# Optimization experiments

Hardware: AMD Instinct MI355X
Metric: run time of the kernel (lower is better)

Reference implementation:

```python
import jax, jax.numpy as jnp
import numpy as np

VAR0, VAR1 = 0.1, 0.2
THRESHOLD = 0.35
NEGPOS_RATIO = 7
LOW_GT_THRESH = 0.2  # match() filters GT whose best prior IoU < 0.2


def setup_inputs() -> dict:
    key = jax.random.key(0)
    ks = jax.random.split(key, 8)
    B, P, G = 16, 43008, 128
    loc_data = jax.random.normal(ks[0], (B, P, 4), jnp.float32)
    conf_data = jax.random.normal(ks[1], (B, P, 2), jnp.float32)
    landm_data = jax.random.normal(ks[2], (B, P, 10), jnp.float32)
    # priors in cxcywh form, positive sizes
    pc = jax.random.uniform(ks[3], (P, 2), jnp.float32)
    pwh = jax.random.uniform(ks[4], (P, 2), jnp.float32, minval=0.02, maxval=0.32)
    priors = jnp.concatenate([pc, pwh], axis=1)
    # targets: valid xyxy boxes + 10 landmark coords + label (face=1)
    ctr = jax.random.uniform(ks[5], (B, G, 2), jnp.float32, minval=0.2, maxval=0.8)
    wh = jax.random.uniform(ks[6], (B, G, 2), jnp.float32, minval=0.05, maxval=0.3)
    boxes = jnp.concatenate([ctr - wh / 2, ctr + wh / 2], axis=-1)
    landms = jax.random.uniform(ks[7], (B, G, 10), jnp.float32)
    labels = jnp.ones((B, G, 1), jnp.float32)
    targets = jnp.concatenate([boxes, landms, labels], axis=-1)
    return {"loc_data": loc_data, "conf_data": conf_data, "landm_data": landm_data,
            "priors": priors, "targets": targets}


def point_form(priors):
    return jnp.concatenate([priors[:, :2] - priors[:, 2:] / 2,
                            priors[:, :2] + priors[:, 2:] / 2], axis=1)


def jaccard(a, b):  # a: [G,4] xyxy, b: [P,4] xyxy -> [G,P]
    lt = jnp.maximum(a[:, None, :2], b[None, :, :2])
    rb = jnp.minimum(a[:, None, 2:], b[None, :, 2:])
    wh = jnp.clip(rb - lt, 0.0)
    inter = wh[..., 0] * wh[..., 1]
    area_a = (a[:, 2] - a[:, 0]) * (a[:, 3] - a[:, 1])
    area_b = (b[:, 2] - b[:, 0]) * (b[:, 3] - b[:, 1])
    return inter / (area_a[:, None] + area_b[None, :] - inter)


def encode(matched, priors):  # matched xyxy [P,4], priors cxcywh [P,4]
    g_cxcy = (matched[:, :2] + matched[:, 2:]) / 2 - priors[:, :2]
    g_cxcy = g_cxcy / (VAR0 * priors[:, 2:])
    g_wh = jnp.log((matched[:, 2:] - matched[:, :2]) / priors[:, 2:]) / VAR1
    return jnp.concatenate([g_cxcy, g_wh], axis=1)


def encode_landm(matched, priors):  # matched [P,10], priors [P,4]
    m = matched.reshape(-1, 5, 2)
    g = (m - priors[:, None, :2]) / (VAR0 * priors[:, None, 2:])
    return g.reshape(-1, 10)


def match_one(truths, labels, landms, priors):
    G = truths.shape[0]
    overlaps = jaccard(truths, point_form(priors))  # [G, P]
    best_prior_overlap = overlaps.max(axis=1)       # [G]
    best_prior_idx = overlaps.argmax(axis=1)        # [G]
    valid = best_prior_overlap >= LOW_GT_THRESH
    any_valid = jnp.any(valid)
    best_truth_overlap = overlaps.max(axis=0)       # [P]
    best_truth_idx = overlaps.argmax(axis=0)        # [P]
    # index_fill_(0, best_prior_idx_filter, 2): ensure each valid GT keeps its best prior
    fill_val = jnp.where(valid, 2.0, best_truth_overlap[best_prior_idx])
    best_truth_overlap = best_truth_overlap.at[best_prior_idx].set(fill_val)
    # best_truth_idx[best_prior_idx[j]] = j for all j
    best_truth_idx = best_truth_idx.at[best_prior_idx].set(jnp.arange(G))
    matches = truths[best_truth_idx]                       # [P,4]
    conf = labels[best_truth_idx].astype(jnp.int32)        # [P]
    conf = jnp.where(best_truth_overlap < THRESHOLD, 0, conf)
    conf = jnp.where(any_valid, conf, 0)  # no valid GT -> all background
    loc = encode(matches, priors)
    landm = encode_landm(landms[best_truth_idx], priors)
    return loc, conf, landm


def smooth_l1(x):
    ax = jnp.abs(x)
    return jnp.where(ax < 1.0, 0.5 * ax * ax, ax - 0.5)


def reference(loc_data, conf_data, landm_data, priors, targets):
    truths = targets[..., :4]
    landms = targets[..., 4:14]
    labels = targets[..., 14]
    loc_t, conf_t, landm_t = jax.vmap(
        lambda t, l, lm: match_one(t, l, lm, priors))(truths, labels, landms)

    # landmark loss over positives
    pos1 = conf_t > 0
    N1 = jnp.maximum(pos1.sum().astype(jnp.float32), 1.0)
    loss_landm = jnp.sum(smooth_l1(landm_data - landm_t) * pos1[..., None])

    # localization loss over positives
    pos = conf_t != 0
    num_pos = pos.sum(axis=1, keepdims=True)  # [B,1]
    loss_l = jnp.sum(smooth_l1(loc_data - loc_t) * pos[..., None])

    # hard negative mining on per-prior CE loss
    lse = jax.scipy.special.logsumexp(conf_data, axis=-1)  # [B,P]
    gathered = jnp.take_along_axis(conf_data, conf_t[..., None], axis=-1)[..., 0]
    ce_all = lse - gathered                                # [B,P] per-prior CE
    mine = jnp.where(pos, 0.0, ce_all)
    loss_idx = jnp.argsort(-mine, axis=1)
    idx_rank = jnp.argsort(loss_idx, axis=1)
    num_neg = jnp.clip(NEGPOS_RATIO * num_pos, None, pos.shape[1] - 1)
    neg = idx_rank < num_neg
    sel = pos | neg
    loss_c = jnp.sum(jnp.where(sel, ce_all, 0.0))

    N = jnp.maximum(num_pos.sum().astype(jnp.float32), 1.0)
    return loss_l / N, loss_c / N, loss_landm / N1
```

## Files before the change

### kernel.cpp

```cpp
#include <hip/hip_runtime.h>
#include <stdint.h>


#define GC 8
#define PPI 4

__device__ __forceinline__ float sl1(float x) {
  float a = fabsf(x);
  return a < 1.f ? 0.5f * a * a : a - 0.5f;
}

__device__ __forceinline__ double dwave(double v) {
#pragma unroll
  for (int o = 32; o; o >>= 1) v += __shfl_down(v, o);
  return v;
}

__global__ __launch_bounds__(256) void k_match(
    const float* __restrict__ priors, const float* __restrict__ targets,
    float* __restrict__ bto, int* __restrict__ bti,
    unsigned long long* __restrict__ bp, int P, int G, int NIOU, int PTI,
    int NGC, int PC) {
  int tid = threadIdx.x;
  __shared__ float4 sgt[128];
  __shared__ float sga[128];
  __shared__ unsigned long long sred[GC * 256];

  if ((int)blockIdx.x < NIOU) {
    int b = blockIdx.x / PTI, tile = blockIdx.x % PTI;
    int base = tile * (256 * PPI);
    for (int g = tid; g < G; g += 256) {
      const float* t = targets + ((size_t)b * G + g) * 15;
      float x1 = t[0], y1 = t[1], x2 = t[2], y2 = t[3];
      sgt[g] = make_float4(x1, y1, x2, y2);
      sga[g] = (x2 - x1) * (y2 - y1);
    }
    __syncthreads();

    float px1[PPI], py1[PPI], px2[PPI], py2[PPI], pa[PPI];
    float bi[PPI], sb[PPI];
    int bidx[PPI];
#pragma unroll
    for (int k = 0; k < PPI; ++k) {
      int p = base + tid + k * 256;
      int pl = p < P ? p : P - 1;
      float4 pr = ((const float4*)priors)[pl];
      px1[k] = pr.x - pr.z * 0.5f; py1[k] = pr.y - pr.w * 0.5f;
      px2[k] = pr.x + pr.z * 0.5f; py2[k] = pr.y + pr.w * 0.5f;
      pa[k] = pr.z * pr.w;
      bi[k] = 0.f; sb[k] = 1.f; bidx[k] = 0;
    }

#define IOU_BODY(T, A, GG)                                                 \
  {                                                                        \
    float iw = fminf(T.z, px2[k]) - fmaxf(T.x, px1[k]);                    \
    float ih = fminf(T.w, py2[k]) - fmaxf(T.y, py1[k]);                    \
    float inter = fmaxf(iw, 0.f) * ih;        \
    float S = A + pa[k];                                                   \
    if (inter * sb[k] > bi[k] * S) { bi[k] = inter; sb[k] = S; bidx[k] = GG; } \
  }

    for (int g = 0; g < G; g += 4) {
      float4 T0 = sgt[g], T1 = sgt[g + 1], T2 = sgt[g + 2], T3 = sgt[g + 3];
      float A0 = sga[g], A1 = sga[g + 1], A2 = sga[g + 2], A3 = sga[g + 3];
#pragma unroll
      for (int k = 0; k < PPI; ++k) {
        IOU_BODY(T0, A0, g)
        IOU_BODY(T1, A1, g + 1)
        IOU_BODY(T2, A2, g + 2)
        IOU_BODY(T3, A3, g + 3)
      }
    }
#undef IOU_BODY
#pragma unroll
    for (int k = 0; k < PPI; ++k) {
      int p = base + tid + k * 256;
      if (p < P) {
        bto[(size_t)b * P + p] = bi[k] / (sb[k] - bi[k]);
        bti[(size_t)b * P + p] = bidx[k];
      }
    }
  } else {
    int bc = blockIdx.x - NIOU;
    int pc = bc % PC;
    int gcb = (bc / PC) % NGC;
    int b = bc / (PC * NGC);
    int g0 = gcb * GC;

    if (tid < GC) {
      int g = g0 + tid;
      float4 v = make_float4(0.f, 0.f, 0.f, 0.f);
      if (g < G) {
        const float* t = targets + ((size_t)b * G + g) * 15;
        v = make_float4(t[0], t[1], t[2], t[3]);
      }
      sgt[tid] = v;
    }
    __syncthreads();

    float gx1[GC], gy1[GC], gx2[GC], gy2[GC], ga[GC];
#pragma unroll
    for (int j = 0; j < GC; ++j) {
      float4 T = sgt[j];
      gx1[j] = T.x; gy1[j] = T.y; gx2[j] = T.z; gy2[j] = T.w;
      ga[j] = (T.z - T.x) * (T.w - T.y);
    }

    int chunk = (P + PC - 1) / PC;
    int ps = pc * chunk;
    int pe = ps + chunk; if (pe > P) pe = P;
    int count = pe - ps;

    float bi[GC], sb[GC];
    unsigned bpp[GC];
#pragma unroll
    for (int j = 0; j < GC; ++j) { bi[j] = 0.f; sb[j] = 1.f; bpp[j] = (unsigned)(ps + tid); }

#define BP_BODY(X1, Y1, X2, Y2, AR, PP)                                     \
  {                                                                         \
    float iw = fminf(gx2[j], X2) - fmaxf(gx1[j], X1);                       \
    float ih = fminf(gy2[j], Y2) - fmaxf(gy1[j], Y1);                       \
    float inter = fmaxf(iw, 0.f) * ih;                                      \
    float S = ga[j] + AR;                                                   \
    if (inter * sb[j] > bi[j] * S) { bi[j] = inter; sb[j] = S; bpp[j] = (unsigned)PP; } \
  }

    for (int i = tid; i < count; i += 1024) {
      int p0 = ps + i;
      int i1 = i + 256, i2 = i + 512, i3 = i + 768;
      int p1 = (i1 < count) ? ps + i1 : p0;
      int p2 = (i2 < count) ? ps + i2 : p0;
      int p3 = (i3 < count) ? ps + i3 : p0;
      float4 q0 = ((const float4*)priors)[p0];
      float4 q1 = ((const float4*)priors)[p1];
      float4 q2 = ((const float4*)priors)[p2];
      float4 q3 = ((const float4*)priors)[p3];
      float ax1 = q0.x - q0.z * 0.5f, ay1 = q0.y - q0.w * 0.5f;
      float ax2 = q0.x + q0.z * 0.5f, ay2 = q0.y + q0.w * 0.5f;
      float aa = q0.z * q0.w;
      float bx1 = q1.x - q1.z * 0.5f, by1 = q1.y - q1.w * 0.5f;
      float bx2 = q1.x + q1.z * 0.5f, by2 = q1.y + q1.w * 0.5f;
      float ba = q1.z * q1.w;
      float cx1 = q2.x - q2.z * 0.5f, cy1 = q2.y - q2.w * 0.5f;
      float cx2 = q2.x + q2.z * 0.5f, cy2 = q2.y + q2.w * 0.5f;
      float ca = q2.z * q2.w;
      float dx1 = q3.x - q3.z * 0.5f, dy1 = q3.y - q3.w * 0.5f;
      float dx2 = q3.x + q3.z * 0.5f, dy2 = q3.y + q3.w * 0.5f;
      float da = q3.z * q3.w;
#pragma unroll
      for (int j = 0; j < GC; ++j) {
        BP_BODY(ax1, ay1, ax2, ay2, aa, p0)
        BP_BODY(bx1, by1, bx2, by2, ba, p1)
        BP_BODY(cx1, cy1, cx2, cy2, ca, p2)
        BP_BODY(dx1, dy1, dx2, dy2, da, p3)
      }
    }
#undef BP_BODY

#pragma unroll
    for (int j = 0; j < GC; ++j) {
      float iou = bi[j] / (sb[j] - bi[j]);
      unsigned long long pk =
          ((unsigned long long)__float_as_uint(iou) << 32) | (unsigned)(~bpp[j]);
      sred[j * 256 + tid] = pk;
    }
    __syncthreads();
    {
      int j = tid >> 5, s = tid & 31;
      unsigned long long m = sred[j * 256 + s];
#pragma unroll
      for (int t = 1; t < 8; ++t) {
        unsigned long long v = sred[j * 256 + s + t * 32];
        if (v > m) m = v;
      }
      __syncthreads();
      sred[j * 256 + s] = m;
    }
    __syncthreads();
    if (tid < GC) {
      unsigned long long m = sred[tid * 256];
      for (int s = 1; s < 32; ++s) {
        unsigned long long v = sred[tid * 256 + s];
        if (v > m) m = v;
      }
      int g = g0 + tid;
      if (g < G) atomicMax(&bp[(size_t)b * G + g], m);
    }
  }
}

__global__ void k_scatter(const unsigned long long* __restrict__ bp,
                          float* __restrict__ bto, int* __restrict__ bti,
                          int* __restrict__ anyv, int P, int G) {
  int b = blockIdx.x, g = threadIdx.x;
  __shared__ unsigned spp[128];
  __shared__ int s_any;
  if (g == 0) s_any = 0;
  __syncthreads();
  unsigned long long m = bp[(size_t)b * G + g];
  unsigned pp = ~(unsigned)m;
  float val = __uint_as_float((unsigned)(m >> 32));
  bool ok = (m != 0ULL);
  float oldv = 0.f;
  if (ok) oldv = bto[(size_t)b * P + pp];
  spp[g] = ok ? pp : 0xFFFFFFFFu;
  if (ok && val >= 0.2f) s_any = 1;
  __syncthreads();
  bool win = ok;
  for (int g2 = g + 1; g2 < G; ++g2)
    if (spp[g2] == pp) win = false;
  if (win) {
    bto[(size_t)b * P + pp] = (val >= 0.2f) ? 2.0f : oldv;
    bti[(size_t)b * P + pp] = g;
  }
  __syncthreads();
  if (g == 0) anyv[b] = s_any;
}

__global__ __launch_bounds__(256) void k_main(
    const float* __restrict__ loc, const float* __restrict__ conf,
    const float* __restrict__ lm, const float* __restrict__ priors,
    const float* __restrict__ targets, const float* __restrict__ bto,
    const int* __restrict__ bti, const int* __restrict__ anyv,
    float* __restrict__ mine, unsigned* __restrict__ h1,
    double* __restrict__ pll, double* __restrict__ pllm,
    double* __restrict__ plc, double* __restrict__ msum,
    int* __restrict__ pnp, int P, int G, int PT) {
  int b = blockIdx.x / PT, tile = blockIdx.x % PT;
  int tid = threadIdx.x;
  int p = tile * 256 + tid;

  __shared__ float st[128 * 15];
  __shared__ unsigned hist[1024];
  __shared__ double rs[16];
  __shared__ int ri[4];

  for (int i = tid; i < G * 15; i += 256) st[i] = targets[(size_t)b * G * 15 + i];
  for (int i = tid; i < 1024; i += 256) hist[i] = 0;
  __syncthreads();

  double ll = 0, llm = 0, lc = 0, ms = 0;
  int np = 0;
  if (p < P) {
    size_t idx = (size_t)b * P + p;
    int av = anyv[b];
    float ov = bto[idx];
    int ti = bti[idx];
    bool pos = av && (ov >= 0.35f);

    float2 c = ((const float2*)conf)[idx];
    float mx = fmaxf(c.x, c.y);
    float lse = mx + logf(expf(c.x - mx) + expf(c.y - mx));
    float ce = lse - (pos ? c.y : c.x);
    float mv = pos ? 0.f : ce;
    mine[idx] = mv;
    ms = (double)mv;
    atomicAdd(&hist[__float_as_uint(mv) >> 21], 1u);

    if (pos) {
      np = 1;
      lc = (double)ce;
      float4 pr = ((const float4*)priors)[p];
      const float* t = st + ti * 15;
      float dx = 0.1f * pr.z, dy = 0.1f * pr.w;
      float gx = ((t[0] + t[2]) * 0.5f - pr.x) / dx;
      float gy = ((t[1] + t[3]) * 0.5f - pr.y) / dy;
      float gw = logf((t[2] - t[0]) / pr.z) * 5.0f;
      float gh = logf((t[3] - t[1]) / pr.w) * 5.0f;
      float4 ld = ((const float4*)loc)[idx];
      ll = (double)(sl1(ld.x - gx) + sl1(ld.y - gy) + sl1(ld.z - gw) +
                    sl1(ld.w - gh));
      const float2* lmd = (const float2*)lm + idx * 5;
      float s = 0.f;
#pragma unroll
      for (int j = 0; j < 5; ++j) {
        float2 lv = lmd[j];
        float ex = (t[4 + 2 * j] - pr.x) / dx;
        float ey = (t[5 + 2 * j] - pr.y) / dy;
        s += sl1(lv.x - ex) + sl1(lv.y - ey);
      }
      llm = (double)s;
    }
  }

  ll = dwave(ll);
  llm = dwave(llm);
  lc = dwave(lc);
  ms = dwave(ms);
#pragma unroll
  for (int o = 32; o; o >>= 1) np += __shfl_down(np, o);
  int lane = tid & 63, wid = tid >> 6;
  if (lane == 0) {
    rs[wid] = ll; rs[4 + wid] = llm; rs[8 + wid] = lc; rs[12 + wid] = ms;
    ri[wid] = np;
  }
  __syncthreads();
  if (tid == 0) {
    pll[blockIdx.x] = rs[0] + rs[1] + rs[2] + rs[3];
    pllm[blockIdx.x] = rs[4] + rs[5] + rs[6] + rs[7];
    plc[blockIdx.x] = rs[8] + rs[9] + rs[10] + rs[11];
    msum[blockIdx.x] = rs[12] + rs[13] + rs[14] + rs[15];
    pnp[blockIdx.x] = ri[0] + ri[1] + ri[2] + ri[3];
  }
  for (int i = tid; i < 1024; i += 256)
    if (hist[i]) atomicAdd(&h1[(size_t)b * 1024 + i], hist[i]);
}

__global__ __launch_bounds__(1024) void k_tail(
    const unsigned* __restrict__ h1, const int* __restrict__ pnp,
    const double* __restrict__ msum, const float* __restrict__ mine,
    int* __restrict__ num_pos, double* __restrict__ pfs_b, int P, int PT) {
  int b = blockIdx.x, tid = threadIdx.x;
  __shared__ double sm[1024];
  __shared__ int sn[1024];
  __shared__ unsigned S[1024];
  __shared__ unsigned hs[2048];
  __shared__ int spf1, sk1, spf21, sk2;
  __shared__ unsigned stb;
  __shared__ double stie;
  __shared__ double rs[16];

  int n = 0;
  double m = 0;
  for (int i = tid; i < PT; i += 1024) { n += pnp[b * PT + i]; m += msum[b * PT + i]; }
  sn[tid] = n; sm[tid] = m;
  __syncthreads();
  for (int off = 512; off; off >>= 1) {
    if (tid < off) { sn[tid] += sn[tid + off]; sm[tid] += sm[tid + off]; }
    __syncthreads();
  }
  int npos = sn[0];
  if (tid == 0) num_pos[b] = npos;

  long long k = 7LL * (long long)npos;
  long long cap = P - 1;
  if (k <= 0) return;
  if (k >= cap) {
    if (tid == 0) pfs_b[b] = sm[0];
    return;
  }

  const float* mrow = mine + (size_t)b * P;

  {
    unsigned own = h1[(size_t)b * 1024 + tid];
    S[tid] = own;
    __syncthreads();
    for (int off = 1; off < 1024; off <<= 1) {
      unsigned add = (tid + off < 1024) ? S[tid + off] : 0;
      __syncthreads();
      S[tid] += add;
      __syncthreads();
    }
    int cnt = __syncthreads_count((long long)S[tid] >= k);
    int seg = cnt - 1;
    if (tid == seg) {
      long long cum = (seg + 1 < 1024) ? (long long)S[seg + 1] : 0;
      spf1 = seg;
      sk1 = (int)(k - cum);
    }
  }
  __syncthreads();
  int pf = spf1;

  hs[tid] = 0; hs[tid + 1024] = 0;
  __syncthreads();
  for (int base = 0; base < P; base += 4096) {
    int i0 = base + tid;
    int i1 = i0 + 1024, i2 = i0 + 2048, i3 = i0 + 3072;
    unsigned b0 = (i0 < P) ? __float_as_uint(mrow[i0]) : 0u;
    unsigned b1 = (i1 < P) ? __float_as_uint(mrow[i1]) : 0u;
    unsigned b2 = (i2 < P) ? __float_as_uint(mrow[i2]) : 0u;
    unsigned b3 = (i3 < P) ? __float_as_uint(mrow[i3]) : 0u;
    if (i0 < P && (int)(b0 >> 21) == pf) atomicAdd(&hs[(b0 >> 10) & 2047], 1u);
    if (i1 < P && (int)(b1 >> 21) == pf) atomicAdd(&hs[(b1 >> 10) & 2047], 1u);
    if (i2 < P && (int)(b2 >> 21) == pf) atomicAdd(&hs[(b2 >> 10) & 2047], 1u);
    if (i3 < P && (int)(b3 >> 21) == pf) atomicAdd(&hs[(b3 >> 10) & 2047], 1u);
  }
  __syncthreads();
  {
    unsigned h0 = hs[tid * 2], h1v = hs[tid * 2 + 1];
    S[tid] = h0 + h1v;
    __syncthreads();
    for (int off = 1; off < 1024; off <<= 1) {
      unsigned add = (tid + off < 1024) ? S[tid + off] : 0;
      __syncthreads();
      S[tid] += add;
      __syncthreads();
    }
    long long kk = (long long)sk1;
    int cnt = __syncthreads_count((long long)S[tid] >= kk);
    int seg = cnt - 1;
    if (tid == seg) {
      long long cum = (seg + 1 < 1024) ? (long long)S[seg + 1] : 0;
      int bin = seg * 2;
      if (cum + h1v >= kk) bin = seg * 2 + 1;
      else cum += h1v;
      spf21 = (pf << 11) | bin;
      sk2 = (int)(kk - cum);
    }
  }
  __syncthreads();
  int pf21 = spf21;

  hs[tid] = 0;
  __syncthreads();
  for (int base = 0; base < P; base += 4096) {
    int i0 = base + tid;
    int i1 = i0 + 1024, i2 = i0 + 2048, i3 = i0 + 3072;
    unsigned b0 = (i0 < P) ? __float_as_uint(mrow[i0]) : 0u;
    unsigned b1 = (i1 < P) ? __float_as_uint(mrow[i1]) : 0u;
    unsigned b2 = (i2 < P) ? __float_as_uint(mrow[i2]) : 0u;
    unsigned b3 = (i3 < P) ? __float_as_uint(mrow[i3]) : 0u;
    if (i0 < P && (int)(b0 >> 10) == pf21) atomicAdd(&hs[b0 & 1023], 1u);
    if (i1 < P && (int)(b1 >> 10) == pf21) atomicAdd(&hs[b1 & 1023], 1u);
    if (i2 < P && (int)(b2 >> 10) == pf21) atomicAdd(&hs[b2 & 1023], 1u);
    if (i3 < P && (int)(b3 >> 10) == pf21) atomicAdd(&hs[b3 & 1023], 1u);
  }
  __syncthreads();
  {
    unsigned own = hs[tid];
    S[tid] = own;
    __syncthreads();
    for (int off = 1; off < 1024; off <<= 1) {
      unsigned add = (tid + off < 1024) ? S[tid + off] : 0;
      __syncthreads();
      S[tid] += add;
      __syncthreads();
    }
    long long kk = (long long)sk2;
    int cnt = __syncthreads_count((long long)S[tid] >= kk);
    int seg = cnt - 1;
    if (tid == seg) {
      long long cum = (seg + 1 < 1024) ? (long long)S[seg + 1] : 0;
      unsigned tb = ((unsigned)pf21 << 10) | (unsigned)seg;
      stb = tb;
      stie = (double)(kk - cum) * (double)__uint_as_float(tb);
    }
  }
  __syncthreads();

  unsigned tb = stb;
  double v = 0.0;
  for (int base = 0; base < P; base += 4096) {
    int i0 = base + tid;
    int i1 = i0 + 1024, i2 = i0 + 2048, i3 = i0 + 3072;
    unsigned b0 = (i0 < P) ? __float_as_uint(mrow[i0]) : 0u;
    unsigned b1 = (i1 < P) ? __float_as_uint(mrow[i1]) : 0u;
    unsigned b2 = (i2 < P) ? __float_as_uint(mrow[i2]) : 0u;
    unsigned b3 = (i3 < P) ? __float_as_uint(mrow[i3]) : 0u;
    if (b0 > tb) v += (double)__uint_as_float(b0);
    if (b1 > tb) v += (double)__uint_as_float(b1);
    if (b2 > tb) v += (double)__uint_as_float(b2);
    if (b3 > tb) v += (double)__uint_as_float(b3);
  }
  v = dwave(v);
  int lane = tid & 63, wid = tid >> 6;
  if (lane == 0) rs[wid] = v;
  __syncthreads();
  if (tid == 0) {
    double t = 0;
    for (int i = 0; i < 16; ++i) t += rs[i];
    pfs_b[b] = t + stie;
  }
}

__global__ __launch_bounds__(256) void k_fin(
    const double* __restrict__ pll, const double* __restrict__ pllm,
    const double* __restrict__ plc, const double* __restrict__ pfs_b,
    const int* __restrict__ num_pos, float* __restrict__ out, int NBm, int B) {
  int tid = threadIdx.x;
  double a = 0, c = 0, d = 0, f = 0, n = 0;
  for (int i = tid; i < NBm; i += 256) { a += pll[i]; c += pllm[i]; d += plc[i]; }
  for (int i = tid; i < B; i += 256) { f += pfs_b[i]; n += (double)num_pos[i]; }
  a = dwave(a); c = dwave(c); d = dwave(d); f = dwave(f); n = dwave(n);
  __shared__ double rs[5 * 4];
  int lane = tid & 63, wid = tid >> 6;
  if (lane == 0) {
    rs[wid] = a; rs[4 + wid] = c; rs[8 + wid] = d;
    rs[12 + wid] = f; rs[16 + wid] = n;
  }
  __syncthreads();
  if (tid == 0) {
    double A = rs[0] + rs[1] + rs[2] + rs[3];
    double C = rs[4] + rs[5] + rs[6] + rs[7];
    double D = rs[8] + rs[9] + rs[10] + rs[11];
    double F = rs[12] + rs[13] + rs[14] + rs[15];
    double N = rs[16] + rs[17] + rs[18] + rs[19];
    if (N < 1.0) N = 1.0;
    out[0] = (float)(A / N);
    out[1] = (float)((D + F) / N);
    out[2] = (float)(C / N);
  }
}

extern "C" void kernel_launch(void* const* d_in, const int* in_sizes, int n_in,
                              void* d_out, int out_size, void* d_ws,
                              size_t ws_size, hipStream_t stream) {
  const float* loc = (const float*)d_in[0];
  const float* conf = (const float*)d_in[1];
  const float* lm = (const float*)d_in[2];
  const float* priors = (const float*)d_in[3];
  const float* targets = (const float*)d_in[4];

  int P = in_sizes[3] / 4;
  int B = in_sizes[0] / (4 * P);
  int G = in_sizes[4] / (15 * B);
  int PT = (P + 255) / 256;
  int PTI = (P + 256 * PPI - 1) / (256 * PPI);
  int NBm = B * PT;
  int NGC = (G + GC - 1) / GC;
  int PC = 8;
  int NIOU = B * PTI;
  int NBP = B * NGC * PC;

  char* w = (char*)d_ws;
  size_t off = 0;
  unsigned long long* bp = (unsigned long long*)(w + off);
  off += (size_t)B * G * 8;
  double* pfs_b = (double*)(w + off);
  off += (size_t)B * 8;
  int* ctrl = (int*)(w + off);
  off += (size_t)(2 * B) * 4;
  int* anyv = ctrl;
  int* num_pos = ctrl + B;
  unsigned* h1 = (unsigned*)(w + off);
  off += (size_t)B * 1024 * 4;
  size_t clear_bytes = off;
  off = (off + 255) & ~(size_t)255;
  float* bto = (float*)(w + off);
  off += (size_t)B * P * 4;
  int* bti = (int*)(w + off);
  off += (size_t)B * P * 4;
  float* mine = (float*)(w + off);
  off += (size_t)B * P * 4;
  double* pll = (double*)(w + off);
  off += (size_t)NBm * 8;
  double* pllm = (double*)(w + off);
  off += (size_t)NBm * 8;
  double* plc = (double*)(w + off);
  off += (size_t)NBm * 8;
  double* msum = (double*)(w + off);
  off += (size_t)NBm * 8;
  int* pnp = (int*)(w + off);
  off += (size_t)NBm * 4;

  hipMemsetAsync(d_ws, 0, clear_bytes, stream);

  k_match<<<NIOU + NBP, 256, 0, stream>>>(priors, targets, bto, bti, bp, P, G,
                                          NIOU, PTI, NGC, PC);
  k_scatter<<<B, G, 0, stream>>>(bp, bto, bti, anyv, P, G);
  k_main<<<B * PT, 256, 0, stream>>>(loc, conf, lm, priors, targets, bto, bti,
                                     anyv, mine, h1, pll, pllm, plc, msum, pnp,
                                     P, G, PT);
  k_tail<<<B, 1024, 0, stream>>>(h1, pnp, msum, mine, num_pos, pfs_b, P, PT);
  k_fin<<<1, 256, 0, stream>>>(pll, pllm, plc, pfs_b, num_pos, (float*)d_out,
                               NBm, B);
}
```

Before: 178.8 us.

## Split match kernel, fuse final reduction into tail, cheapen per-prior math

```diff
diff --git a/kernel.cpp b/kernel.cpp
--- a/kernel.cpp
+++ b/kernel.cpp
@@ -3,7 +3,7 @@
 
 
 #define GC 8
-#define PPI 4
+#define PPI 2
 
 __device__ __forceinline__ float sl1(float x) {
   float a = fabsf(x);
@@ -16,40 +16,36 @@
   return v;
 }
 
-__global__ __launch_bounds__(256) void k_match(
+__global__ __launch_bounds__(256) void k_iou(
     const float* __restrict__ priors, const float* __restrict__ targets,
-    float* __restrict__ bto, int* __restrict__ bti,
-    unsigned long long* __restrict__ bp, int P, int G, int NIOU, int PTI,
-    int NGC, int PC) {
+    float* __restrict__ bto, int* __restrict__ bti, int P, int G, int PTI) {
   int tid = threadIdx.x;
   __shared__ float4 sgt[128];
   __shared__ float sga[128];
-  __shared__ unsigned long long sred[GC * 256];
-
-  if ((int)blockIdx.x < NIOU) {
-    int b = blockIdx.x / PTI, tile = blockIdx.x % PTI;
-    int base = tile * (256 * PPI);
-    for (int g = tid; g < G; g += 256) {
-      const float* t = targets + ((size_t)b * G + g) * 15;
-      float x1 = t[0], y1 = t[1], x2 = t[2], y2 = t[3];
-      sgt[g] = make_float4(x1, y1, x2, y2);
-      sga[g] = (x2 - x1) * (y2 - y1);
-    }
-    __syncthreads();
-
-    float px1[PPI], py1[PPI], px2[PPI], py2[PPI], pa[PPI];
-    float bi[PPI], sb[PPI];
-    int bidx[PPI];
-#pragma unroll
-    for (int k = 0; k < PPI; ++k) {
-      int p = base + tid + k * 256;
-      int pl = p < P ? p : P - 1;
-      float4 pr = ((const float4*)priors)[pl];
-      px1[k] = pr.x - pr.z * 0.5f; py1[k] = pr.y - pr.w * 0.5f;
-      px2[k] = pr.x + pr.z * 0.5f; py2[k] = pr.y + pr.w * 0.5f;
-      pa[k] = pr.z * pr.w;
-      bi[k] = 0.f; sb[k] = 1.f; bidx[k] = 0;
-    }
+
+  int b = blockIdx.x / PTI, tile = blockIdx.x % PTI;
+  int base = tile * (256 * PPI);
+  for (int g = tid; g < G; g += 256) {
+    const float* t = targets + ((size_t)b * G + g) * 15;
+    float x1 = t[0], y1 = t[1], x2 = t[2], y2 = t[3];
+    sgt[g] = make_float4(x1, y1, x2, y2);
+    sga[g] = (x2 - x1) * (y2 - y1);
+  }
+  __syncthreads();
+
+  float px1[PPI], py1[PPI], px2[PPI], py2[PPI], pa[PPI];
+  float bi[PPI], sb[PPI];
+  int bidx[PPI];
+#pragma unroll
+  for (int k = 0; k < PPI; ++k) {
+    int p = base + tid + k * 256;
+    int pl = p < P ? p : P - 1;
+    float4 pr = ((const float4*)priors)[pl];
+    px1[k] = pr.x - pr.z * 0.5f; py1[k] = pr.y - pr.w * 0.5f;
+    px2[k] = pr.x + pr.z * 0.5f; py2[k] = pr.y + pr.w * 0.5f;
+    pa[k] = pr.z * pr.w;
+    bi[k] = 0.f; sb[k] = 1.f; bidx[k] = 0;
+  }
 
 #define IOU_BODY(T, A, GG)                                                 \
   {                                                                        \
@@ -60,61 +56,69 @@
     if (inter * sb[k] > bi[k] * S) { bi[k] = inter; sb[k] = S; bidx[k] = GG; } \
   }
 
-    for (int g = 0; g < G; g += 4) {
-      float4 T0 = sgt[g], T1 = sgt[g + 1], T2 = sgt[g + 2], T3 = sgt[g + 3];
-      float A0 = sga[g], A1 = sga[g + 1], A2 = sga[g + 2], A3 = sga[g + 3];
-#pragma unroll
-      for (int k = 0; k < PPI; ++k) {
-        IOU_BODY(T0, A0, g)
-        IOU_BODY(T1, A1, g + 1)
-        IOU_BODY(T2, A2, g + 2)
-        IOU_BODY(T3, A3, g + 3)
-      }
-    }
+  for (int g = 0; g < G; g += 4) {
+    float4 T0 = sgt[g], T1 = sgt[g + 1], T2 = sgt[g + 2], T3 = sgt[g + 3];
+    float A0 = sga[g], A1 = sga[g + 1], A2 = sga[g + 2], A3 = sga[g + 3];
+#pragma unroll
+    for (int k = 0; k < PPI; ++k) {
+      IOU_BODY(T0, A0, g)
+      IOU_BODY(T1, A1, g + 1)
+      IOU_BODY(T2, A2, g + 2)
+      IOU_BODY(T3, A3, g + 3)
+    }
+  }
 #undef IOU_BODY
 #pragma unroll
-    for (int k = 0; k < PPI; ++k) {
-      int p = base + tid + k * 256;
-      if (p < P) {
-        bto[(size_t)b * P + p] = bi[k] / (sb[k] - bi[k]);
-        bti[(size_t)b * P + p] = bidx[k];
-      }
-    }
-  } else {
-    int bc = blockIdx.x - NIOU;
-    int pc = bc % PC;
-    int gcb = (bc / PC) % NGC;
-    int b = bc / (PC * NGC);
-    int g0 = gcb * GC;
-
-    if (tid < GC) {
-      int g = g0 + tid;
-      float4 v = make_float4(0.f, 0.f, 0.f, 0.f);
-      if (g < G) {
-        const float* t = targets + ((size_t)b * G + g) * 15;
-        v = make_float4(t[0], t[1], t[2], t[3]);
-      }
-      sgt[tid] = v;
-    }
-    __syncthreads();
-
-    float gx1[GC], gy1[GC], gx2[GC], gy2[GC], ga[GC];
-#pragma unroll
-    for (int j = 0; j < GC; ++j) {
-      float4 T = sgt[j];
-      gx1[j] = T.x; gy1[j] = T.y; gx2[j] = T.z; gy2[j] = T.w;
-      ga[j] = (T.z - T.x) * (T.w - T.y);
-    }
-
-    int chunk = (P + PC - 1) / PC;
-    int ps = pc * chunk;
-    int pe = ps + chunk; if (pe > P) pe = P;
-    int count = pe - ps;
-
-    float bi[GC], sb[GC];
-    unsigned bpp[GC];
-#pragma unroll
-    for (int j = 0; j < GC; ++j) { bi[j] = 0.f; sb[j] = 1.f; bpp[j] = (unsigned)(ps + tid); }
+  for (int k = 0; k < PPI; ++k) {
+    int p = base + tid + k * 256;
+    if (p < P) {
+      bto[(size_t)b * P + p] = bi[k] / (sb[k] - bi[k]);
+      bti[(size_t)b * P + p] = bidx[k];
+    }
+  }
+}
+
+__global__ __launch_bounds__(256) void k_bp(
+    const float* __restrict__ priors, const float* __restrict__ targets,
+    unsigned long long* __restrict__ bp, int P, int G, int NGC, int PC) {
+  int tid = threadIdx.x;
+  __shared__ float4 sgt[GC];
+  __shared__ unsigned long long sred[GC * 256];
+
+  int bc = blockIdx.x;
+  int pc = bc % PC;
+  int gcb = (bc / PC) % NGC;
+  int b = bc / (PC * NGC);
+  int g0 = gcb * GC;
+
+  if (tid < GC) {
+    int g = g0 + tid;
+    float4 v = make_float4(0.f, 0.f, 0.f, 0.f);
+    if (g < G) {
+      const float* t = targets + ((size_t)b * G + g) * 15;
+      v = make_float4(t[0], t[1], t[2], t[3]);
+    }
+    sgt[tid] = v;
+  }
+  __syncthreads();
+
+  float gx1[GC], gy1[GC], gx2[GC], gy2[GC], ga[GC];
+#pragma unroll
+  for (int j = 0; j < GC; ++j) {
+    float4 T = sgt[j];
+    gx1[j] = T.x; gy1[j] = T.y; gx2[j] = T.z; gy2[j] = T.w;
+    ga[j] = (T.z - T.x) * (T.w - T.y);
+  }
+
+  int chunk = (P + PC - 1) / PC;
+  int ps = pc * chunk;
+  int pe = ps + chunk; if (pe > P) pe = P;
+  int count = pe - ps;
+
+  float bi[GC], sb[GC];
+  unsigned bpp[GC];
+#pragma unroll
+  for (int j = 0; j < GC; ++j) { bi[j] = 0.f; sb[j] = 1.f; bpp[j] = (unsigned)(ps + tid); }
 
 #define BP_BODY(X1, Y1, X2, Y2, AR, PP)                                     \
   {                                                                         \
@@ -125,67 +129,66 @@
     if (inter * sb[j] > bi[j] * S) { bi[j] = inter; sb[j] = S; bpp[j] = (unsigned)PP; } \
   }
 
-    for (int i = tid; i < count; i += 1024) {
-      int p0 = ps + i;
-      int i1 = i + 256, i2 = i + 512, i3 = i + 768;
-      int p1 = (i1 < count) ? ps + i1 : p0;
-      int p2 = (i2 < count) ? ps + i2 : p0;
-      int p3 = (i3 < count) ? ps + i3 : p0;
-      float4 q0 = ((const float4*)priors)[p0];
-      float4 q1 = ((const float4*)priors)[p1];
-      float4 q2 = ((const float4*)priors)[p2];
-      float4 q3 = ((const float4*)priors)[p3];
-      float ax1 = q0.x - q0.z * 0.5f, ay1 = q0.y - q0.w * 0.5f;
-      float ax2 = q0.x + q0.z * 0.5f, ay2 = q0.y + q0.w * 0.5f;
-      float aa = q0.z * q0.w;
-      float bx1 = q1.x - q1.z * 0.5f, by1 = q1.y - q1.w * 0.5f;
-      float bx2 = q1.x + q1.z * 0.5f, by2 = q1.y + q1.w * 0.5f;
-      float ba = q1.z * q1.w;
-      float cx1 = q2.x - q2.z * 0.5f, cy1 = q2.y - q2.w * 0.5f;
-      float cx2 = q2.x + q2.z * 0.5f, cy2 = q2.y + q2.w * 0.5f;
-      float ca = q2.z * q2.w;
-      float dx1 = q3.x - q3.z * 0.5f, dy1 = q3.y - q3.w * 0.5f;
-      float dx2 = q3.x + q3.z * 0.5f, dy2 = q3.y + q3.w * 0.5f;
-      float da = q3.z * q3.w;
-#pragma unroll
-      for (int j = 0; j < GC; ++j) {
-        BP_BODY(ax1, ay1, ax2, ay2, aa, p0)
-        BP_BODY(bx1, by1, bx2, by2, ba, p1)
-        BP_BODY(cx1, cy1, cx2, cy2, ca, p2)
-        BP_BODY(dx1, dy1, dx2, dy2, da, p3)
-      }
-    }
+  for (int i = tid; i < count; i += 1024) {
+    int p0 = ps + i;
+    int i1 = i + 256, i2 = i + 512, i3 = i + 768;
+    int p1 = (i1 < count) ? ps + i1 : p0;
+    int p2 = (i2 < count) ? ps + i2 : p0;
+    int p3 = (i3 < count) ? ps + i3 : p0;
+    float4 q0 = ((const float4*)priors)[p0];
+    float4 q1 = ((const float4*)priors)[p1];
+    float4 q2 = ((const float4*)priors)[p2];
+    float4 q3 = ((const float4*)priors)[p3];
+    float ax1 = q0.x - q0.z * 0.5f, ay1 = q0.y - q0.w * 0.5f;
+    float ax2 = q0.x + q0.z * 0.5f, ay2 = q0.y + q0.w * 0.5f;
+    float aa = q0.z * q0.w;
+    float bx1 = q1.x - q1.z * 0.5f, by1 = q1.y - q1.w * 0.5f;
+    float bx2 = q1.x + q1.z * 0.5f, by2 = q1.y + q1.w * 0.5f;
+    float ba = q1.z * q1.w;
+    float cx1 = q2.x - q2.z * 0.5f, cy1 = q2.y - q2.w * 0.5f;
+    float cx2 = q2.x + q2.z * 0.5f, cy2 = q2.y + q2.w * 0.5f;
+    float ca = q2.z * q2.w;
+    float dx1 = q3.x - q3.z * 0.5f, dy1 = q3.y - q3.w * 0.5f;
+    float dx2 = q3.x + q3.z * 0.5f, dy2 = q3.y + q3.w * 0.5f;
+    float da = q3.z * q3.w;
+#pragma unroll
+    for (int j = 0; j < GC; ++j) {
+      BP_BODY(ax1, ay1, ax2, ay2, aa, p0)
+      BP_BODY(bx1, by1, bx2, by2, ba, p1)
+      BP_BODY(cx1, cy1, cx2, cy2, ca, p2)
+      BP_BODY(dx1, dy1, dx2, dy2, da, p3)
+    }
+  }
 #undef BP_BODY
 
 #pragma unroll
-    for (int j = 0; j < GC; ++j) {
-      float iou = bi[j] / (sb[j] - bi[j]);
-      unsigned long long pk =
-          ((unsigned long long)__float_as_uint(iou) << 32) | (unsigned)(~bpp[j]);
-      sred[j * 256 + tid] = pk;
-    }
-    __syncthreads();
-    {
-      int j = tid >> 5, s = tid & 31;
-      unsigned long long m = sred[j * 256 + s];
-#pragma unroll
-      for (int t = 1; t < 8; ++t) {
-        unsigned long long v = sred[j * 256 + s + t * 32];
-        if (v > m) m = v;
-      }
-      __syncthreads();
-      sred[j * 256 + s] = m;
-    }
-    __syncthreads();
-    if (tid < GC) {
-      unsigned long long m = sred[tid * 256];
-      for (int s = 1; s < 32; ++s) {
-        unsigned long long v = sred[tid * 256 + s];
-        if (v > m) m = v;
-      }
-      int g = g0 + tid;
-      if (g < G) atomicMax(&bp[(size_t)b * G + g], m);
-    }
+  for (int j = 0; j < GC; ++j) {
+    float iou = bi[j] / (sb[j] - bi[j]);
+    unsigned long long pk =
+        ((unsigned long long)__float_as_uint(iou) << 32) | (unsigned)(~bpp[j]);
+    sred[j * 256 + tid] = pk;
+  }
+  __syncthreads();
+  {
+    int j = tid >> 5, s = tid & 31;
+    unsigned long long m = sred[j * 256 + s];
+#pragma unroll
+    for (int t = 1; t < 8; ++t) {
+      unsigned long long v = sred[j * 256 + s + t * 32];
+      if (v > m) m = v;
+    }
+    __syncthreads();
+    sred[j * 256 + s] = m;
+  }
+  __syncthreads();
+  if (tid < GC) {
+    unsigned long long m = sred[tid * 256];
+    for (int s = 1; s < 32; ++s) {
+      unsigned long long v = sred[tid * 256 + s];
+      if (v > m) m = v;
+    }
+    int g = g0 + tid;
+    if (g < G) atomicMax(&bp[(size_t)b * G + g], m);
   }
 }
 
@@ -250,7 +253,8 @@
 
     float2 c = ((const float2*)conf)[idx];
     float mx = fmaxf(c.x, c.y);
-    float lse = mx + logf(expf(c.x - mx) + expf(c.y - mx));
+    float d = fabsf(c.x - c.y);
+    float lse = mx + logf(1.f + expf(-d));
     float ce = lse - (pos ? c.y : c.x);
     float mv = pos ? 0.f : ce;
     mine[idx] = mv;
@@ -262,11 +266,12 @@
       lc = (double)ce;
       float4 pr = ((const float4*)priors)[p];
       const float* t = st + ti * 15;
-      float dx = 0.1f * pr.z, dy = 0.1f * pr.w;
-      float gx = ((t[0] + t[2]) * 0.5f - pr.x) / dx;
-      float gy = ((t[1] + t[3]) * 0.5f - pr.y) / dy;
-      float gw = logf((t[2] - t[0]) / pr.z) * 5.0f;
-      float gh = logf((t[3] - t[1]) / pr.w) * 5.0f;
+      float rz = 1.f / pr.z, rw = 1.f / pr.w;
+      float rdx = 10.f * rz, rdy = 10.f * rw;
+      float gx = ((t[0] + t[2]) * 0.5f - pr.x) * rdx;
+      float gy = ((t[1] + t[3]) * 0.5f - pr.y) * rdy;
+      float gw = logf((t[2] - t[0]) * rz) * 5.0f;
+      float gh = logf((t[3] - t[1]) * rw) * 5.0f;
       float4 ld = ((const float4*)loc)[idx];
       ll = (double)(sl1(ld.x - gx) + sl1(ld.y - gy) + sl1(ld.z - gw) +
                     sl1(ld.w - gh));
@@ -275,8 +280,8 @@
 #pragma unroll
       for (int j = 0; j < 5; ++j) {
         float2 lv = lmd[j];
-        float ex = (t[4 + 2 * j] - pr.x) / dx;
-        float ey = (t[5 + 2 * j] - pr.y) / dy;
+        float ex = (t[4 + 2 * j] - pr.x) * rdx;
+        float ey = (t[5 + 2 * j] - pr.y) * rdy;
         s += sl1(lv.x - ex) + sl1(lv.y - ey);
       }
       llm = (double)s;
@@ -309,7 +314,10 @@
 __global__ __launch_bounds__(1024) void k_tail(
     const unsigned* __restrict__ h1, const int* __restrict__ pnp,
     const double* __restrict__ msum, const float* __restrict__ mine,
-    int* __restrict__ num_pos, double* __restrict__ pfs_b, int P, int PT) {
+    const double* __restrict__ pll, const double* __restrict__ pllm,
+    const double* __restrict__ plc, int* __restrict__ num_pos,
+    double* __restrict__ pfs_b, int* __restrict__ ctr,
+    float* __restrict__ out, int P, int PT, int NBm, int B) {
   int b = blockIdx.x, tid = threadIdx.x;
   __shared__ double sm[1024];
   __shared__ int sn[1024];
@@ -319,6 +327,7 @@
   __shared__ unsigned stb;
   __shared__ double stie;
   __shared__ double rs[16];
+  __shared__ int slast;
 
   int n = 0;
   double m = 0;
@@ -334,159 +343,161 @@
 
   long long k = 7LL * (long long)npos;
   long long cap = P - 1;
-  if (k <= 0) return;
-  if (k >= cap) {
-    if (tid == 0) pfs_b[b] = sm[0];
-    return;
-  }
-
-  const float* mrow = mine + (size_t)b * P;
-
-  {
-    unsigned own = h1[(size_t)b * 1024 + tid];
-    S[tid] = own;
-    __syncthreads();
-    for (int off = 1; off < 1024; off <<= 1) {
-      unsigned add = (tid + off < 1024) ? S[tid + off] : 0;
+  double result = 0.0;
+  if (k > 0 && k >= cap) {
+    result = sm[0];
+  } else if (k > 0) {
+    const float* mrow = mine + (size_t)b * P;
+    {
+      unsigned own = h1[(size_t)b * 1024 + tid];
+      S[tid] = own;
       __syncthreads();
-      S[tid] += add;
+      for (int off = 1; off < 1024; off <<= 1) {
+        unsigned add = (tid + off < 1024) ? S[tid + off] : 0;
+        __syncthreads();
+        S[tid] += add;
+        __syncthreads();
+      }
+      int cnt = __syncthreads_count((long long)S[tid] >= k);
+      int seg = cnt - 1;
+      if (tid == seg) {
+        long long cum = (seg + 1 < 1024) ? (long long)S[seg + 1] : 0;
+        spf1 = seg;
+        sk1 = (int)(k - cum);
+      }
+    }
+    __syncthreads();
+    int pf = spf1;
+
+    hs[tid] = 0; hs[tid + 1024] = 0;
+    __syncthreads();
+    for (int base = 0; base < P; base += 4096) {
+      int i0 = base + tid;
+      int i1 = i0 + 1024, i2 = i0 + 2048, i3 = i0 + 3072;
+      unsigned b0 = (i0 < P) ? __float_as_uint(mrow[i0]) : 0u;
+      unsigned b1 = (i1 < P) ? __float_as_uint(mrow[i1]) : 0u;
+      unsigned b2 = (i2 < P) ? __float_as_uint(mrow[i2]) : 0u;
+      unsigned b3 = (i3 < P) ? __float_as_uint(mrow[i3]) : 0u;
+      if (i0 < P && (int)(b0 >> 21) == pf) atomicAdd(&hs[(b0 >> 10) & 2047], 1u);
+      if (i1 < P && (int)(b1 >> 21) == pf) atomicAdd(&hs[(b1 >> 10) & 2047], 1u);
+      if (i2 < P && (int)(b2 >> 21) == pf) atomicAdd(&hs[(b2 >> 10) & 2047], 1u);
+      if (i3 < P && (int)(b3 >> 21) == pf) atomicAdd(&hs[(b3 >> 10) & 2047], 1u);
+    }
+    __syncthreads();
+    {
+      unsigned h0 = hs[tid * 2], h1v = hs[tid * 2 + 1];
+      S[tid] = h0 + h1v;
       __syncthreads();
-    }
-    int cnt = __syncthreads_count((long long)S[tid] >= k);
-    int seg = cnt - 1;
-    if (tid == seg) {
-      long long cum = (seg + 1 < 1024) ? (long long)S[seg + 1] : 0;
-      spf1 = seg;
-      sk1 = (int)(k - cum);
-    }
-  }
-  __syncthreads();
-  int pf = spf1;
-
-  hs[tid] = 0; hs[tid + 1024] = 0;
-  __syncthreads();
-  for (int base = 0; base < P; base += 4096) {
-    int i0 = base + tid;
-    int i1 = i0 + 1024, i2 = i0 + 2048, i3 = i0 + 3072;
-    unsigned b0 = (i0 < P) ? __float_as_uint(mrow[i0]) : 0u;
-    unsigned b1 = (i1 < P) ? __float_as_uint(mrow[i1]) : 0u;
-    unsigned b2 = (i2 < P) ? __float_as_uint(mrow[i2]) : 0u;
-    unsigned b3 = (i3 < P) ? __float_as_uint(mrow[i3]) : 0u;
-    if (i0 < P && (int)(b0 >> 21) == pf) atomicAdd(&hs[(b0 >> 10) & 2047], 1u);
-    if (i1 < P && (int)(b1 >> 21) == pf) atomicAdd(&hs[(b1 >> 10) & 2047], 1u);
-    if (i2 < P && (int)(b2 >> 21) == pf) atomicAdd(&hs[(b2 >> 10) & 2047], 1u);
-    if (i3 < P && (int)(b3 >> 21) == pf) atomicAdd(&hs[(b3 >> 10) & 2047], 1u);
-  }
-  __syncthreads();
-  {
-    unsigned h0 = hs[tid * 2], h1v = hs[tid * 2 + 1];
-    S[tid] = h0 + h1v;
-    __syncthreads();
-    for (int off = 1; off < 1024; off <<= 1) {
-      unsigned add = (tid + off < 1024) ? S[tid + off] : 0;
+      for (int off = 1; off < 1024; off <<= 1) {
+        unsigned add = (tid + off < 1024) ? S[tid + off] : 0;
+        __syncthreads();
+        S[tid] += add;
+        __syncthreads();
+      }
+      long long kk = (long long)sk1;
+      int cnt = __syncthreads_count((long long)S[tid] >= kk);
+      int seg = cnt - 1;
+      if (tid == seg) {
+        long long cum = (seg + 1 < 1024) ? (long long)S[seg + 1] : 0;
+        int bin = seg * 2;
+        if (cum + h1v >= kk) bin = seg * 2 + 1;
+        else cum += h1v;
+        spf21 = (pf << 11) | bin;
+        sk2 = (int)(kk - cum);
+      }
+    }
+    __syncthreads();
+    int pf21 = spf21;
+
+    hs[tid] = 0;
+    __syncthreads();
+    for (int base = 0; base < P; base += 4096) {
+      int i0 = base + tid;
+      int i1 = i0 + 1024, i2 = i0 + 2048, i3 = i0 + 3072;
+      unsigned b0 = (i0 < P) ? __float_as_uint(mrow[i0]) : 0u;
+      unsigned b1 = (i1 < P) ? __float_as_uint(mrow[i1]) : 0u;
+      unsigned b2 = (i2 < P) ? __float_as_uint(mrow[i2]) : 0u;
+      unsigned b3 = (i3 < P) ? __float_as_uint(mrow[i3]) : 0u;
+      if (i0 < P && (int)(b0 >> 10) == pf21) atomicAdd(&hs[b0 & 1023], 1u);
+      if (i1 < P && (int)(b1 >> 10) == pf21) atomicAdd(&hs[b1 & 1023], 1u);
+      if (i2 < P && (int)(b2 >> 10) == pf21) atomicAdd(&hs[b2 & 1023], 1u);
+      if (i3 < P && (int)(b3 >> 10) == pf21) atomicAdd(&hs[b3 & 1023], 1u);
+    }
+    __syncthreads();
+    {
+      unsigned own = hs[tid];
+      S[tid] = own;
       __syncthreads();
-      S[tid] += add;
-      __syncthreads();
-    }
-    long long kk = (long long)sk1;
-    int cnt = __syncthreads_count((long long)S[tid] >= kk);
-    int seg = cnt - 1;
-    if (tid == seg) {
-      long long cum = (seg + 1 < 1024) ? (long long)S[seg + 1] : 0;
-      int bin = seg * 2;
-      if (cum + h1v >= kk) bin = seg * 2 + 1;
-      else cum += h1v;
-      spf21 = (pf << 11) | bin;
-      sk2 = (int)(kk - cum);
-    }
-  }
-  __syncthreads();
-  int pf21 = spf21;
-
-  hs[tid] = 0;
-  __syncthreads();
-  for (int base = 0; base < P; base += 4096) {
-    int i0 = base + tid;
-    int i1 = i0 + 1024, i2 = i0 + 2048, i3 = i0 + 3072;
-    unsigned b0 = (i0 < P) ? __float_as_uint(mrow[i0]) : 0u;
-    unsigned b1 = (i1 < P) ? __float_as_uint(mrow[i1]) : 0u;
-    unsigned b2 = (i2 < P) ? __float_as_uint(mrow[i2]) : 0u;
-    unsigned b3 = (i3 < P) ? __float_as_uint(mrow[i3]) : 0u;
-    if (i0 < P && (int)(b0 >> 10) == pf21) atomicAdd(&hs[b0 & 1023], 1u);
-    if (i1 < P && (int)(b1 >> 10) == pf21) atomicAdd(&hs[b1 & 1023], 1u);
-    if (i2 < P && (int)(b2 >> 10) == pf21) atomicAdd(&hs[b2 & 1023], 1u);
-    if (i3 < P && (int)(b3 >> 10) == pf21) atomicAdd(&hs[b3 & 1023], 1u);
-  }
-  __syncthreads();
-  {
-    unsigned own = hs[tid];
-    S[tid] = own;
-    __syncthreads();
-    for (int off = 1; off < 1024; off <<= 1) {
-      unsigned add = (tid + off < 1024) ? S[tid + off] : 0;
-      __syncthreads();
-      S[tid] += add;
-      __syncthreads();
-    }
-    long long kk = (long long)sk2;
-    int cnt = __syncthreads_count((long long)S[tid] >= kk);
-    int seg = cnt - 1;
-    if (tid == seg) {
-      long long cum = (seg + 1 < 1024) ? (long long)S[seg + 1] : 0;
-      unsigned tb = ((unsigned)pf21 << 10) | (unsigned)seg;
-      stb = tb;
-      stie = (double)(kk - cum) * (double)__uint_as_float(tb);
-    }
-  }
-  __syncthreads();
-
-  unsigned tb = stb;
-  double v = 0.0;
-  for (int base = 0; base < P; base += 4096) {
-    int i0 = base + tid;
-    int i1 = i0 + 1024, i2 = i0 + 2048, i3 = i0 + 3072;
-    unsigned b0 = (i0 < P) ? __float_as_uint(mrow[i0]) : 0u;
-    unsigned b1 = (i1 < P) ? __float_as_uint(mrow[i1]) : 0u;
-    unsigned b2 = (i2 < P) ? __float_as_uint(mrow[i2]) : 0u;
-    unsigned b3 = (i3 < P) ? __float_as_uint(mrow[i3]) : 0u;
-    if (b0 > tb) v += (double)__uint_as_float(b0);
-    if (b1 > tb) v += (double)__uint_as_float(b1);
-    if (b2 > tb) v += (double)__uint_as_float(b2);
-    if (b3 > tb) v += (double)__uint_as_float(b3);
-  }
-  v = dwave(v);
-  int lane = tid & 63, wid = tid >> 6;
-  if (lane == 0) rs[wid] = v;
+      for (int off = 1; off < 1024; off <<= 1) {
+        unsigned add = (tid + off < 1024) ? S[tid + off] : 0;
+        __syncthreads();
+        S[tid] += add;
+        __syncthreads();
+      }
+      long long kk = (long long)sk2;
+      int cnt = __syncthreads_count((long long)S[tid] >= kk);
+      int seg = cnt - 1;
+      if (tid == seg) {
+        long long cum = (seg + 1 < 1024) ? (long long)S[seg + 1] : 0;
+        unsigned tb = ((unsigned)pf21 << 10) | (unsigned)seg;
+        stb = tb;
+        stie = (double)(kk - cum) * (double)__uint_as_float(tb);
+      }
+    }
+    __syncthreads();
+
+    unsigned tb = stb;
+    double v = 0.0;
+    for (int base = 0; base < P; base += 4096) {
+      int i0 = base + tid;
+      int i1 = i0 + 1024, i2 = i0 + 2048, i3 = i0 + 3072;
+      unsigned b0 = (i0 < P) ? __float_as_uint(mrow[i0]) : 0u;
+      unsigned b1 = (i1 < P) ? __float_as_uint(mrow[i1]) : 0u;
+      unsigned b2 = (i2 < P) ? __float_as_uint(mrow[i2]) : 0u;
+      unsigned b3 = (i3 < P) ? __float_as_uint(mrow[i3]) : 0u;
+      if (b0 > tb) v += (double)__uint_as_float(b0);
+      if (b1 > tb) v += (double)__uint_as_float(b1);
+      if (b2 > tb) v += (double)__uint_as_float(b2);
+      if (b3 > tb) v += (double)__uint_as_float(b3);
+    }
+    v = dwave(v);
+    int lane = tid & 63, wid = tid >> 6;
+    if (lane == 0) rs[wid] = v;
+    __syncthreads();
+    if (tid == 0) {
+      double t = 0;
+      for (int i = 0; i < 16; ++i) t += rs[i];
+      result = t + stie;
+    }
+  }
+  if (tid == 0) pfs_b[b] = result;
+
   __syncthreads();
   if (tid == 0) {
-    double t = 0;
-    for (int i = 0; i < 16; ++i) t += rs[i];
-    pfs_b[b] = t + stie;
-  }
-}
-
-__global__ __launch_bounds__(256) void k_fin(
-    const double* __restrict__ pll, const double* __restrict__ pllm,
-    const double* __restrict__ plc, const double* __restrict__ pfs_b,
-    const int* __restrict__ num_pos, float* __restrict__ out, int NBm, int B) {
-  int tid = threadIdx.x;
-  double a = 0, c = 0, d = 0, f = 0, n = 0;
-  for (int i = tid; i < NBm; i += 256) { a += pll[i]; c += pllm[i]; d += plc[i]; }
-  for (int i = tid; i < B; i += 256) { f += pfs_b[i]; n += (double)num_pos[i]; }
-  a = dwave(a); c = dwave(c); d = dwave(d); f = dwave(f); n = dwave(n);
-  __shared__ double rs[5 * 4];
+    __threadfence();
+    slast = (atomicAdd(ctr, 1) == B - 1) ? 1 : 0;
+  }
+  __syncthreads();
+  if (!slast) return;
+  __threadfence();
+
+  double a = 0, c = 0, d2 = 0, f = 0, n2 = 0;
+  for (int i = tid; i < NBm; i += 1024) { a += pll[i]; c += pllm[i]; d2 += plc[i]; }
+  for (int i = tid; i < B; i += 1024) { f += pfs_b[i]; n2 += (double)num_pos[i]; }
+  a = dwave(a); c = dwave(c); d2 = dwave(d2); f = dwave(f); n2 = dwave(n2);
+  __shared__ double fr[5 * 16];
   int lane = tid & 63, wid = tid >> 6;
   if (lane == 0) {
-    rs[wid] = a; rs[4 + wid] = c; rs[8 + wid] = d;
-    rs[12 + wid] = f; rs[16 + wid] = n;
+    fr[wid] = a; fr[16 + wid] = c; fr[32 + wid] = d2;
+    fr[48 + wid] = f; fr[64 + wid] = n2;
   }
   __syncthreads();
   if (tid == 0) {
-    double A = rs[0] + rs[1] + rs[2] + rs[3];
-    double C = rs[4] + rs[5] + rs[6] + rs[7];
-    double D = rs[8] + rs[9] + rs[10] + rs[11];
-    double F = rs[12] + rs[13] + rs[14] + rs[15];
-    double N = rs[16] + rs[17] + rs[18] + rs[19];
+    double A = 0, C = 0, D = 0, F = 0, N = 0;
+    for (int i = 0; i < 16; ++i) {
+      A += fr[i]; C += fr[16 + i]; D += fr[32 + i];
+      F += fr[48 + i]; N += fr[64 + i];
+    }
     if (N < 1.0) N = 1.0;
     out[0] = (float)(A / N);
     out[1] = (float)((D + F) / N);
@@ -511,8 +522,6 @@
   int NBm = B * PT;
   int NGC = (G + GC - 1) / GC;
   int PC = 8;
-  int NIOU = B * PTI;
-  int NBP = B * NGC * PC;
 
   char* w = (char*)d_ws;
   size_t off = 0;
@@ -521,9 +530,11 @@
   double* pfs_b = (double*)(w + off);
   off += (size_t)B * 8;
   int* ctrl = (int*)(w + off);
-  off += (size_t)(2 * B) * 4;
+  off += (size_t)(2 * B + 2) * 4;
   int* anyv = ctrl;
   int* num_pos = ctrl + B;
+  int* ctr = ctrl + 2 * B;
+  off = (off + 7) & ~(size_t)7;
   unsigned* h1 = (unsigned*)(w + off);
   off += (size_t)B * 1024 * 4;
   size_t clear_bytes = off;
@@ -547,13 +558,12 @@
 
   hipMemsetAsync(d_ws, 0, clear_bytes, stream);
 
-  k_match<<<NIOU + NBP, 256, 0, stream>>>(priors, targets, bto, bti, bp, P, G,
-                                          NIOU, PTI, NGC, PC);
+  k_iou<<<B * PTI, 256, 0, stream>>>(priors, targets, bto, bti, P, G, PTI);
+  k_bp<<<B * NGC * PC, 256, 0, stream>>>(priors, targets, bp, P, G, NGC, PC);
   k_scatter<<<B, G, 0, stream>>>(bp, bto, bti, anyv, P, G);
   k_main<<<B * PT, 256, 0, stream>>>(loc, conf, lm, priors, targets, bto, bti,
                                      anyv, mine, h1, pll, pllm, plc, msum, pnp,
                                      P, G, PT);
-  k_tail<<<B, 1024, 0, stream>>>(h1, pnp, msum, mine, num_pos, pfs_b, P, PT);
-  k_fin<<<1, 256, 0, stream>>>(pll, pllm, plc, pfs_b, num_pos, (float*)d_out,
-                               NBm, B);
-}
+  k_tail<<<B, 1024, 0, stream>>>(h1, pnp, msum, mine, pll, pllm, plc, num_pos,
+                                 pfs_b, ctr, (float*)d_out, P, PT, NBm, B);
+}
```

Result: slower. 194.8 us (+9.0%).
